# Optimization experiments

Measured on AMD Instinct MI355X. Metric: run time of the kernel, lower is better.

The kernel has to match this reference:

```python
import jax, jax.numpy as jnp
import numpy as np

RNN = 64      # rnn_hidden_dim
HID = 64      # hidden_dim
ENC = 3       # encoder_dim
NAG = 8       # n_agents
NACT = 14     # n_actions
CLIP = 0.2    # args.exp_clip (variance floor)
BN_EPS = 1e-5


def _bn(x, g, b):
    # BatchNorm1d in training mode: batch stats, biased variance
    m = x.mean(0)
    v = jnp.mean((x - m) ** 2, 0)
    return g * (x - m) * jax.lax.rsqrt(v + BN_EPS) + b


def setup_inputs() -> dict:
    key = jax.random.key(0)
    ks = jax.random.split(key, 16)
    B, INP = 8192, 96

    def w(k, shape, fan):
        return (jax.random.normal(k, shape, jnp.float32) / np.float32(np.sqrt(fan)))

    d = {}
    d["inputs"] = jax.random.normal(ks[0], (B * NAG, INP), jnp.float32)
    d["hidden_state"] = jax.random.normal(ks[1], (B * NAG, RNN), jnp.float32)
    d["noise"] = jax.random.normal(ks[2], (B, NAG, NAG * ENC), jnp.float32)
    d["fc1_w"] = w(ks[3], (INP, RNN), INP); d["fc1_b"] = jnp.zeros((RNN,), jnp.float32)
    d["w_ih"] = w(ks[4], (RNN, 3 * RNN), RNN); d["w_hh"] = w(ks[5], (RNN, 3 * RNN), RNN)
    d["b_ih"] = jnp.zeros((3 * RNN,), jnp.float32); d["b_hh"] = jnp.zeros((3 * RNN,), jnp.float32)
    d["aw1_w"] = w(ks[6], (RNN, HID), RNN); d["aw1_b"] = jnp.zeros((HID,), jnp.float32)
    d["aw_g"] = jnp.ones((HID,), jnp.float32); d["aw_be"] = jnp.zeros((HID,), jnp.float32)
    d["aw2_w"] = w(ks[7], (HID, 2 * NAG * ENC), HID); d["aw2_b"] = jnp.zeros((2 * NAG * ENC,), jnp.float32)
    d["po1_w"] = w(ks[8], (2 * RNN, HID), 2 * RNN); d["po1_b"] = jnp.zeros((HID,), jnp.float32)
    d["po_g"] = jnp.ones((HID,), jnp.float32); d["po_be"] = jnp.zeros((HID,), jnp.float32)
    d["po2_w"] = w(ks[9], (HID, 2 * ENC), HID); d["po2_b"] = jnp.zeros((2 * ENC,), jnp.float32)
    d["fc2_w"] = w(ks[10], (RNN + ENC * NAG, NACT), RNN + ENC * NAG); d["fc2_b"] = jnp.zeros((NACT,), jnp.float32)
    return d


def reference(inputs, hidden_state, noise,
              fc1_w, fc1_b, w_ih, w_hh, b_ih, b_hh,
              aw1_w, aw1_b, aw_g, aw_be, aw2_w, aw2_b,
              po1_w, po1_b, po_g, po_be, po2_w, po2_b,
              fc2_w, fc2_b):
    B, n, enc = noise.shape[0], NAG, ENC

    x = jax.nn.relu(inputs @ fc1_w + fc1_b)                      # [B*n, RNN]
    h_in = hidden_state.reshape(-1, RNN)

    # torch GRUCell
    gi = x @ w_ih + b_ih
    gh = h_in @ w_hh + b_hh
    ir, iz, i_n = jnp.split(gi, 3, axis=-1)
    hr, hz, h_n = jnp.split(gh, 3, axis=-1)
    r = jax.nn.sigmoid(ir + hr)
    z = jax.nn.sigmoid(iz + hz)
    nt = jnp.tanh(i_n + r * h_n)
    h = (1.0 - z) * nt + z * h_in                                # [B*n, RNN]

    # awareness encoder
    a = jax.nn.relu(_bn(h @ aw1_w + aw1_b, aw_g, aw_be))
    aw = (a @ aw2_w + aw2_b).reshape(B, n, 2 * n * enc)
    mu = aw[:, :, : n * enc]
    sigma = jnp.maximum(jnp.exp(aw[:, :, n * enc:]), CLIP)       # variance
    c = (mu + jnp.sqrt(sigma) * noise).reshape(-1, n * enc)      # rsample

    x_out = jnp.concatenate([h, c], axis=-1) @ fc2_w + fc2_b     # [B*n, NACT]

    # poster branch (training mode): all-pairs concat H[b, j, id] = [h[b,id], h[b,j]]
    hd = jax.lax.stop_gradient(h).reshape(B, n, RNN)
    Hi = jnp.broadcast_to(hd[:, None, :, :], (B, n, n, RNN))     # axis2 = id
    Hj = jnp.broadcast_to(hd[:, :, None, :], (B, n, n, RNN))     # axis1 = j
    H = jnp.concatenate([Hi, Hj], axis=-1).reshape(-1, 2 * RNN)  # [B*n*n, 2*RNN]

    p = jax.nn.relu(_bn(H @ po1_w + po1_b, po_g, po_be))
    out = (p @ po2_w + po2_b).reshape(B, n, 2 * n * enc)
    mu1 = out[:, :, : n * enc]
    sigma1 = jnp.maximum(jnp.exp(out[:, :, n * enc:]), CLIP)

    # KL between diagonal Gaussians (sigma, sigma1 are variances)
    kl = 0.5 * (jnp.log(sigma1 / sigma) + (sigma + (mu - mu1) ** 2) / sigma1 - 1.0)
    KL = kl.mean(axis=-1).mean(axis=-1, keepdims=True)           # [B, 1]
    return (x_out, h, KL)
```

## Files before the change

### kernel.cpp

```cpp
#include <hip/hip_runtime.h>
#include <math.h>

#define NROWS 65536
#define NB    8192
#define STAT_OFF  0
#define WPACK_OFF 448
#define OUT_XOUT 0
#define OUT_H    917504
#define OUT_KL   5111808

typedef __attribute__((ext_vector_type(8))) short bhalf8;
typedef __attribute__((ext_vector_type(4))) float floatx4;
typedef __attribute__((ext_vector_type(4))) unsigned short u16x4;

__device__ __forceinline__ float sigmf(float x) { return 1.0f / (1.0f + __expf(-x)); }
__device__ __forceinline__ float tanhfast(float x) {
    x = fminf(fmaxf(x, -15.f), 15.f);
    float e = __expf(-2.f * x);
    return (1.f - e) / (1.f + e);
}
__device__ __forceinline__ unsigned short f2bf(float f) {
    unsigned int u = __float_as_uint(f);
    u += 0x7FFFu + ((u >> 16) & 1u);
    return (unsigned short)(u >> 16);
}
__device__ __forceinline__ float bf2f(unsigned short s) {
    return __uint_as_float(((unsigned int)s) << 16);
}
__device__ __forceinline__ bhalf8 pack8(float4 a, float4 b) {
    bhalf8 r;
    r[0] = (short)f2bf(a.x); r[1] = (short)f2bf(a.y);
    r[2] = (short)f2bf(a.z); r[3] = (short)f2bf(a.w);
    r[4] = (short)f2bf(b.x); r[5] = (short)f2bf(b.y);
    r[6] = (short)f2bf(b.z); r[7] = (short)f2bf(b.w);
    return r;
}

__device__ __forceinline__ int p2idx(int g, int i) {
    switch (i) {
        case 0:  return (0 + g) * 2 + 0;   case 1:  return (0 + g) * 2 + 1;
        case 2:  return (12 + g) * 2 + 0;  case 3:  return (12 + g) * 2 + 1;
        case 4:  return (4 + g) * 2 + 0;   case 5:  return (4 + g) * 2 + 1;
        case 6:  return (16 + g) * 2 + 0;  case 7:  return (16 + g) * 2 + 1;
        case 8:  return (8 + g) * 2 + 0;   case 9:  return (8 + g) * 2 + 1;
        case 10: return (20 + g) * 2 + 0;  default: return (20 + g) * 2 + 1;
    }
}
__device__ __forceinline__ int p3idx(int g, int i) {
    switch (i) {
        case 0: return g * 2 + 0;        case 1: return g * 2 + 1;
        case 2: return (4 + g) * 2 + 0;  case 3: return (4 + g) * 2 + 1;
        case 4: return (8 + g) * 2 + 0;  default: return (8 + g) * 2 + 1;
    }
}

__global__ void k_prep(const float* __restrict__ fc1_w,
                       const float* __restrict__ w_ih, const float* __restrict__ w_hh,
                       const float* __restrict__ aw1_w, const float* __restrict__ po1_w,
                       const float* __restrict__ aw2_w, const float* __restrict__ fc2_w,
                       float* __restrict__ ws)
{
    const int t = threadIdx.x;
    if (blockIdx.x == 0)
        for (int i = t; i < 448; i += 256) ws[STAT_OFF + i] = 0.f;

    unsigned short* wpk = (unsigned short*)(ws + WPACK_OFF);
    for (int f = blockIdx.x * 256 + t; f < 5952; f += gridDim.x * 256) {
        int lane, c, tile;
        const float* src;
        int colbase, krowstride, kofs = 0, kmax = 1 << 30, colmax = 16;
        if (f < 768) {
            tile = f / 192; c = (f % 192) / 64; lane = f % 64;
            src = fc1_w; krowstride = 64; colbase = tile * 16;
        } else if (f < 3840) {
            int f2 = f - 768;
            tile = f2 / 128; c = (f2 % 128) / 64; lane = f2 % 64;
            if (tile < 12) { src = w_ih; colbase = tile * 16; }
            else           { src = w_hh; colbase = (tile - 12) * 16; }
            krowstride = 192;
        } else if (f < 5376) {
            int f3 = f - 3840;
            tile = f3 / 128; c = (f3 % 128) / 64; lane = f3 % 64;
            if (tile < 4)       { src = aw1_w; colbase = tile * 16; }
            else if (tile < 8)  { src = po1_w; colbase = (tile - 4) * 16; }
            else                { src = po1_w; colbase = (tile - 8) * 16; kofs = 64; }
            krowstride = 64;
        } else if (f < 5760) {
            int f4 = f - 5376;
            tile = f4 / 128; c = (f4 % 128) / 64; lane = f4 % 64;
            src = aw2_w; krowstride = 48; colbase = tile * 16;
        } else {
            int f5 = f - 5760;
            c = f5 / 64; lane = f5 % 64;
            src = fc2_w; krowstride = 14; colbase = 0;
            kmax = 88; colmax = 14;
        }
        int n = lane & 15, quad = lane >> 4;
        int col = colbase + n;
        unsigned short o[8];
        #pragma unroll
        for (int j = 0; j < 8; j++) {
            int k = c * 32 + quad * 8 + j + kofs;
            float v = (k < kmax && n < colmax) ? src[(size_t)k * krowstride + col] : 0.f;
            o[j] = f2bf(v);
        }
        u16x4 lo, hi;
        lo.x = o[0]; lo.y = o[1]; lo.z = o[2]; lo.w = o[3];
        hi.x = o[4]; hi.y = o[5]; hi.z = o[6]; hi.w = o[7];
        *(u16x4*)&wpk[f * 8]     = lo;
        *(u16x4*)&wpk[f * 8 + 4] = hi;
    }
}

__global__ __launch_bounds__(256, 2) void k_front(
    const float* __restrict__ inp, const float* __restrict__ hin,
    const float* __restrict__ fc1_b,
    const float* __restrict__ b_ih, const float* __restrict__ b_hh,
    const float* __restrict__ aw1_b,
    float* __restrict__ h_out, float* __restrict__ ws)
{
    __shared__ __align__(16) unsigned short s_xb[128 * 80];
    __shared__ float s_stat[448];

    const int t = threadIdx.x;
    const int row0 = blockIdx.x * 128;
    const int lane = t & 63;
    const int w = t >> 6;
    const int n16 = lane & 15;
    const int quad = lane >> 4;

    for (int i = t; i < 448; i += 256) s_stat[i] = 0.f;
    __syncthreads();

    const bhalf8* wp1 = (const bhalf8*)((const unsigned short*)(ws + WPACK_OFF));
    const bhalf8* wp2 = wp1 + 768;
    const bhalf8* wp3 = wp1 + 3840;

    bhalf8 ai[2][3], ahf[2][2];
    #pragma unroll
    for (int u = 0; u < 2; u++) {
        const float* gi = inp + (size_t)(row0 + w * 32 + u * 16 + n16) * 96 + quad * 8;
        #pragma unroll
        for (int kc = 0; kc < 3; kc++)
            ai[u][kc] = pack8(*(const float4*)&gi[kc * 32], *(const float4*)&gi[kc * 32 + 4]);
        const float* gh = hin + (size_t)(row0 + w * 32 + u * 16 + n16) * 64 + quad * 8;
        #pragma unroll
        for (int kc = 0; kc < 2; kc++)
            ahf[u][kc] = pack8(*(const float4*)&gh[kc * 32], *(const float4*)&gh[kc * 32 + 4]);
    }

    float b1v[4], brv[4], bzv[4], binv[4], bhnv[4], abv[4];
    #pragma unroll
    for (int g = 0; g < 4; g++) {
        int col = g * 16 + n16;
        b1v[g]  = fc1_b[col];
        brv[g]  = b_ih[col] + b_hh[col];
        bzv[g]  = b_ih[64 + col] + b_hh[64 + col];
        binv[g] = b_ih[128 + col];
        bhnv[g] = b_hh[128 + col];
        abv[g]  = aw1_b[col];
    }

    bhalf8 f1a[2][3];
    #pragma unroll
    for (int i = 0; i < 3; i++) f1a[0][i] = wp1[i * 64 + lane];
    #pragma unroll
    for (int g = 0; g < 4; g++) {
        const int cur = g & 1, nxt = cur ^ 1;
        if (g < 3) {
            #pragma unroll
            for (int i = 0; i < 3; i++) f1a[nxt][i] = wp1[((g + 1) * 3 + i) * 64 + lane];
        }
        int col = g * 16 + n16;
        #pragma unroll
        for (int u = 0; u < 2; u++) {
            floatx4 d = {0.f, 0.f, 0.f, 0.f};
            d = __builtin_amdgcn_mfma_f32_16x16x32_bf16(ai[u][0], f1a[cur][0], d, 0, 0, 0);
            d = __builtin_amdgcn_mfma_f32_16x16x32_bf16(ai[u][1], f1a[cur][1], d, 0, 0, 0);
            d = __builtin_amdgcn_mfma_f32_16x16x32_bf16(ai[u][2], f1a[cur][2], d, 0, 0, 0);
            #pragma unroll
            for (int q = 0; q < 4; q++)
                s_xb[(w * 32 + u * 16 + quad * 4 + q) * 80 + col] = f2bf(fmaxf(d[q] + b1v[g], 0.f));
        }
    }

    bhalf8 f2a[2][12];
    float hpv[2][8];
    #pragma unroll
    for (int i = 0; i < 12; i++) f2a[0][i] = wp2[p2idx(0, i) * 64 + lane];
    #pragma unroll
    for (int u = 0; u < 2; u++)
        #pragma unroll
        for (int q = 0; q < 4; q++)
            hpv[0][u * 4 + q] = hin[(size_t)(row0 + w * 32 + u * 16 + quad * 4 + q) * 64 + n16];

    bhalf8 ax[2][2];
    #pragma unroll
    for (int u = 0; u < 2; u++) {
        int mr = w * 32 + u * 16 + n16;
        ax[u][0] = *(const bhalf8*)&s_xb[mr * 80 + 0  + quad * 8];
        ax[u][1] = *(const bhalf8*)&s_xb[mr * 80 + 32 + quad * 8];
    }

    #pragma unroll
    for (int g = 0; g < 4; g++) {
        const int cur = g & 1, nxt = cur ^ 1;
        if (g < 3) {
            #pragma unroll
            for (int i = 0; i < 12; i++) f2a[nxt][i] = wp2[p2idx(g + 1, i) * 64 + lane];
            #pragma unroll
            for (int u = 0; u < 2; u++)
                #pragma unroll
                for (int q = 0; q < 4; q++)
                    hpv[nxt][u * 4 + q] = hin[(size_t)(row0 + w * 32 + u * 16 + quad * 4 + q) * 64 + (g + 1) * 16 + n16];
        }
        int col = g * 16 + n16;
        floatx4 dr[2], dz[2], dn[2], dh[2];
        #pragma unroll
        for (int u = 0; u < 2; u++) {
            floatx4 d = {0.f, 0.f, 0.f, 0.f};
            d = __builtin_amdgcn_mfma_f32_16x16x32_bf16(ax[u][0], f2a[cur][0], d, 0, 0, 0);
            d = __builtin_amdgcn_mfma_f32_16x16x32_bf16(ax[u][1], f2a[cur][1], d, 0, 0, 0);
            d = __builtin_amdgcn_mfma_f32_16x16x32_bf16(ahf[u][0], f2a[cur][2], d, 0, 0, 0);
            d = __builtin_amdgcn_mfma_f32_16x16x32_bf16(ahf[u][1], f2a[cur][3], d, 0, 0, 0);
            dr[u] = d;
            floatx4 e = {0.f, 0.f, 0.f, 0.f};
            e = __builtin_amdgcn_mfma_f32_16x16x32_bf16(ax[u][0], f2a[cur][4], e, 0, 0, 0);
            e = __builtin_amdgcn_mfma_f32_16x16x32_bf16(ax[u][1], f2a[cur][5], e, 0, 0, 0);
            e = __builtin_amdgcn_mfma_f32_16x16x32_bf16(ahf[u][0], f2a[cur][6], e, 0, 0, 0);
            e = __builtin_amdgcn_mfma_f32_16x16x32_bf16(ahf[u][1], f2a[cur][7], e, 0, 0, 0);
            dz[u] = e;
            floatx4 f = {0.f, 0.f, 0.f, 0.f};
            f = __builtin_amdgcn_mfma_f32_16x16x32_bf16(ax[u][0], f2a[cur][8], f, 0, 0, 0);
            f = __builtin_amdgcn_mfma_f32_16x16x32_bf16(ax[u][1], f2a[cur][9], f, 0, 0, 0);
            dn[u] = f;
            floatx4 h4 = {0.f, 0.f, 0.f, 0.f};
            h4 = __builtin_amdgcn_mfma_f32_16x16x32_bf16(ahf[u][0], f2a[cur][10], h4, 0, 0, 0);
            h4 = __builtin_amdgcn_mfma_f32_16x16x32_bf16(ahf[u][1], f2a[cur][11], h4, 0, 0, 0);
            dh[u] = h4;
        }
        #pragma unroll
        for (int u = 0; u < 2; u++) {
            #pragma unroll
            for (int q = 0; q < 4; q++) {
                int lrow = w * 32 + u * 16 + quad * 4 + q;
                size_t grow = (size_t)(row0 + lrow);
                float r  = sigmf(dr[u][q] + brv[g]);
                float z  = sigmf(dz[u][q] + bzv[g]);
                float nt = tanhfast(dn[u][q] + binv[g] + r * (dh[u][q] + bhnv[g]));
                float hp = hpv[cur][u * 4 + q];
                float h  = (1.f - z) * nt + z * hp;
                h_out[grow * 64 + col] = h;
                s_xb[lrow * 80 + col] = f2bf(h);
            }
        }
    }

    bhalf8 f3a[2][6];
    #pragma unroll
    for (int i = 0; i < 6; i++) f3a[0][i] = wp3[p3idx(0, i) * 64 + lane];

    bhalf8 hh[2][2];
    #pragma unroll
    for (int u = 0; u < 2; u++) {
        int mr = w * 32 + u * 16 + n16;
        hh[u][0] = *(const bhalf8*)&s_xb[mr * 80 + 0  + quad * 8];
        hh[u][1] = *(const bhalf8*)&s_xb[mr * 80 + 32 + quad * 8];
    }

    #pragma unroll
    for (int g = 0; g < 4; g++) {
        const int cur = g & 1, nxt = cur ^ 1;
        if (g < 3) {
            #pragma unroll
            for (int i = 0; i < 6; i++) f3a[nxt][i] = wp3[p3idx(g + 1, i) * 64 + lane];
        }
        int col = g * 16 + n16;
        floatx4 da[2], du[2], dvv[2];
        #pragma unroll
        for (int u = 0; u < 2; u++) {
            floatx4 d = {0.f, 0.f, 0.f, 0.f};
            d = __builtin_amdgcn_mfma_f32_16x16x32_bf16(hh[u][0], f3a[cur][0], d, 0, 0, 0);
            d = __builtin_amdgcn_mfma_f32_16x16x32_bf16(hh[u][1], f3a[cur][1], d, 0, 0, 0);
            da[u] = d;
            floatx4 e = {0.f, 0.f, 0.f, 0.f};
            e = __builtin_amdgcn_mfma_f32_16x16x32_bf16(hh[u][0], f3a[cur][2], e, 0, 0, 0);
            e = __builtin_amdgcn_mfma_f32_16x16x32_bf16(hh[u][1], f3a[cur][3], e, 0, 0, 0);
            du[u] = e;
            floatx4 f = {0.f, 0.f, 0.f, 0.f};
            f = __builtin_amdgcn_mfma_f32_16x16x32_bf16(hh[u][0], f3a[cur][4], f, 0, 0, 0);
            f = __builtin_amdgcn_mfma_f32_16x16x32_bf16(hh[u][1], f3a[cur][5], f, 0, 0, 0);
            dvv[u] = f;
        }
        float ab = abv[g];
        float s1 = 0.f, s2 = 0.f, suq = 0.f, svq = 0.f;
        float su[2] = {0.f, 0.f}, sv[2] = {0.f, 0.f};
        #pragma unroll
        for (int u = 0; u < 2; u++) {
            #pragma unroll
            for (int q = 0; q < 4; q++) {
                float a = da[u][q] + ab; s1 += a; s2 += a * a;
                float uv = du[u][q]; su[u] += uv; suq += uv * uv;
                float vv = dvv[u][q]; sv[u] += vv; svq += vv * vv;
            }
        }
        #pragma unroll
        for (int u = 0; u < 2; u++) {
            float u8 = su[u] + __shfl_xor(su[u], 16, 64);
            float v8 = sv[u] + __shfl_xor(sv[u], 16, 64);
            if ((quad & 1) == 0)
                atomicAdd(&s_stat[384 + col], u8 * v8 * (1.f / 64.f));
        }
        float sut = su[0] + su[1];
        float svt = sv[0] + sv[1];
        float t1 = s1 + __shfl_xor(s1, 16, 64);   t1 += __shfl_xor(t1, 32, 64);
        float t2 = s2 + __shfl_xor(s2, 16, 64);   t2 += __shfl_xor(t2, 32, 64);
        float t3 = sut + __shfl_xor(sut, 16, 64); t3 += __shfl_xor(t3, 32, 64);
        float t4 = suq + __shfl_xor(suq, 16, 64); t4 += __shfl_xor(t4, 32, 64);
        float t5 = svt + __shfl_xor(svt, 16, 64); t5 += __shfl_xor(t5, 32, 64);
        float t6 = svq + __shfl_xor(svq, 16, 64); t6 += __shfl_xor(t6, 32, 64);
        if (quad == 0) {
            atomicAdd(&s_stat[col], t1);
            atomicAdd(&s_stat[64 + col], t2);
            atomicAdd(&s_stat[128 + col], t3);
            atomicAdd(&s_stat[192 + col], t4);
            atomicAdd(&s_stat[256 + col], t5);
            atomicAdd(&s_stat[320 + col], t6);
        }
    }
    __syncthreads();
    if (t < 64) {
        float* gs = ws + STAT_OFF;
        #pragma unroll
        for (int q = 0; q < 7; q++)
            atomicAdd(&gs[q * 64 + t], s_stat[q * 64 + t]);
    }
}

__global__ __launch_bounds__(128) void k_heads(
    const float* __restrict__ h_glob, const float* __restrict__ noise,
    const float* __restrict__ aw1_b, const float* __restrict__ aw2_b,
    const float* __restrict__ fc2_b, const float* __restrict__ po2_b,
    const float* __restrict__ aw_g, const float* __restrict__ aw_be,
    const float* __restrict__ po_g, const float* __restrict__ po_be,
    const float* __restrict__ po1_b, const float* __restrict__ po2_w,
    const float* __restrict__ ws, float* __restrict__ out)
{
    __shared__ __align__(16) unsigned short s_hb[32 * 104];
    __shared__ __align__(16) unsigned short s_Ub[32 * 80];
    __shared__ __align__(16) unsigned short s_Vb[32 * 80];
    __shared__ float s_ms[32 * 48];
    __shared__ __align__(16) float s_out[32 * 48];
    __shared__ __align__(16) float s_dv[640];
    __shared__ float s_kl[32];

    const int t = threadIdx.x;
    const int row0 = blockIdx.x * 32;
    const int b0 = blockIdx.x * 4;
    const int lane = t & 63;
    const int w = t >> 6;
    const int n16 = lane & 15;
    const int quad = lane >> 4;
    const int mrow = w * 16 + n16;

    if (t < 64) {
        const float* st = ws + STAT_OFF;
        const float invN = 1.f / 65536.f;
        float am = st[t] * invN;
        float av = st[64 + t] * invN - am * am;
        float asc = aw_g[t] * rsqrtf(av + 1e-5f);
        s_dv[t] = asc;
        s_dv[64 + t] = aw_be[t] - asc * am;
        float Eu = st[128 + t] * invN;
        float vu = st[192 + t] * invN - Eu * Eu;
        float Ev = st[256 + t] * invN;
        float vv = st[320 + t] * invN - Ev * Ev;
        float cov = st[384 + t] * (1.f / 8192.f) - Eu * Ev;
        float my = Eu + Ev + po1_b[t];
        float vy = vu + vv + 2.f * cov;
        float psc = po_g[t] * rsqrtf(vy + 1e-5f);
        s_dv[128 + t] = psc;
        s_dv[192 + t] = po_be[t] + psc * (po1_b[t] - my);
    }
    for (int i = t; i < 384; i += 128) {
        int d = i >> 6, c = i & 63;
        s_dv[256 + i] = po2_w[c * 6 + d];
    }

    {
        const float* gh = h_glob + (size_t)row0 * 64;
        for (int i = t; i < 512; i += 128) {
            int r = i >> 4, c4 = (i & 15) * 4;
            float4 v = *(const float4*)&gh[r * 64 + c4];
            u16x4 p; p.x = f2bf(v.x); p.y = f2bf(v.y); p.z = f2bf(v.z); p.w = f2bf(v.w);
            *(u16x4*)&s_hb[r * 104 + c4] = p;
        }
        for (int i = t; i < 64; i += 128) {
            int r = i >> 1, c4 = 88 + (i & 1) * 4;
            u16x4 z; z.x = 0; z.y = 0; z.z = 0; z.w = 0;
            *(u16x4*)&s_hb[r * 104 + c4] = z;
        }
    }
    __syncthreads();

    const bhalf8* wp3  = ((const bhalf8*)((const unsigned short*)(ws + WPACK_OFF))) + 3840;
    const bhalf8* wpa2 = wp3 + 1536;
    const bhalf8* wpf2 = wpa2 + 384;
    unsigned short* s_ab = (unsigned short*)s_out;

    {
        bhalf8 ah0 = *(const bhalf8*)&s_hb[mrow * 104 + 0  + quad * 8];
        bhalf8 ah1 = *(const bhalf8*)&s_hb[mrow * 104 + 32 + quad * 8];
        #pragma unroll
        for (int g = 0; g < 4; g++) {
            int col = g * 16 + n16;
            floatx4 da = {0.f, 0.f, 0.f, 0.f}, duu = {0.f, 0.f, 0.f, 0.f}, dvv = {0.f, 0.f, 0.f, 0.f};
            da  = __builtin_amdgcn_mfma_f32_16x16x32_bf16(ah0, wp3[(g * 2 + 0) * 64 + lane], da, 0, 0, 0);
            da  = __builtin_amdgcn_mfma_f32_16x16x32_bf16(ah1, wp3[(g * 2 + 1) * 64 + lane], da, 0, 0, 0);
            duu = __builtin_amdgcn_mfma_f32_16x16x32_bf16(ah0, wp3[((4 + g) * 2 + 0) * 64 + lane], duu, 0, 0, 0);
            duu = __builtin_amdgcn_mfma_f32_16x16x32_bf16(ah1, wp3[((4 + g) * 2 + 1) * 64 + lane], duu, 0, 0, 0);
            dvv = __builtin_amdgcn_mfma_f32_16x16x32_bf16(ah0, wp3[((8 + g) * 2 + 0) * 64 + lane], dvv, 0, 0, 0);
            dvv = __builtin_amdgcn_mfma_f32_16x16x32_bf16(ah1, wp3[((8 + g) * 2 + 1) * 64 + lane], dvv, 0, 0, 0);
            float ab = aw1_b[col];
            float asc = s_dv[col], ash = s_dv[64 + col];
            float psc = s_dv[128 + col], psh = s_dv[192 + col];
            #pragma unroll
            for (int q = 0; q < 4; q++) {
                int lrow = w * 16 + quad * 4 + q;
                s_ab[lrow * 80 + col] = f2bf(fmaxf(asc * (da[q] + ab) + ash, 0.f));
                s_Ub[lrow * 80 + col] = f2bf(psc * duu[q]);
                s_Vb[lrow * 80 + col] = f2bf(psc * dvv[q] + psh);
            }
        }
    }

    {
        bhalf8 aa0 = *(const bhalf8*)&s_ab[mrow * 80 + 0  + quad * 8];
        bhalf8 aa1 = *(const bhalf8*)&s_ab[mrow * 80 + 32 + quad * 8];
        #pragma unroll
        for (int g = 0; g < 3; g++) {
            floatx4 d = {0.f, 0.f, 0.f, 0.f};
            d = __builtin_amdgcn_mfma_f32_16x16x32_bf16(aa0, wpa2[(g * 2 + 0) * 64 + lane], d, 0, 0, 0);
            d = __builtin_amdgcn_mfma_f32_16x16x32_bf16(aa1, wpa2[(g * 2 + 1) * 64 + lane], d, 0, 0, 0);
            int col = g * 16 + n16;
            float bb = aw2_b[col];
            #pragma unroll
            for (int q = 0; q < 4; q++) {
                int lrow = w * 16 + quad * 4 + q;
                float v = d[q] + bb;
                s_ms[lrow * 48 + col] = (col < 24) ? v : fmaxf(__expf(v), 0.2f);
            }
        }
    }
    __syncthreads();

    for (int i = t; i < 768; i += 128) {
        int r = i / 24, m = i - r * 24;
        float c = s_ms[r * 48 + m] + sqrtf(s_ms[r * 48 + 24 + m]) * noise[(size_t)(row0 + r) * 24 + m];
        s_hb[r * 104 + 64 + m] = f2bf(c);
    }
    __syncthreads();

    {
        bhalf8 hc0 = *(const bhalf8*)&s_hb[mrow * 104 + 0  + quad * 8];
        bhalf8 hc1 = *(const bhalf8*)&s_hb[mrow * 104 + 32 + quad * 8];
        bhalf8 hc2 = *(const bhalf8*)&s_hb[mrow * 104 + 64 + quad * 8];
        floatx4 d = {0.f, 0.f, 0.f, 0.f};
        d = __builtin_amdgcn_mfma_f32_16x16x32_bf16(hc0, wpf2[0 * 64 + lane], d, 0, 0, 0);
        d = __builtin_amdgcn_mfma_f32_16x16x32_bf16(hc1, wpf2[1 * 64 + lane], d, 0, 0, 0);
        d = __builtin_amdgcn_mfma_f32_16x16x32_bf16(hc2, wpf2[2 * 64 + lane], d, 0, 0, 0);
        if (n16 < 14) {
            float bb = fc2_b[n16];
            float* xout = out + OUT_XOUT;
            #pragma unroll
            for (int q = 0; q < 4; q++) {
                size_t grow = (size_t)(row0 + w * 16 + quad * 4 + q);
                xout[grow * 14 + n16] = d[q] + bb;
            }
        }
    }
    __syncthreads();

    {
        const float* p2t = s_dv + 256;
        const int bl = t >> 5;
        const int rem = t & 31;
        const int i_ = rem >> 2;
        const int j0 = (rem & 3) * 2;
        float acc[2][6];
        #pragma unroll
        for (int jj = 0; jj < 2; jj++)
            #pragma unroll
            for (int d = 0; d < 6; d++) acc[jj][d] = 0.f;

        for (int c = 0; c < 64; c += 4) {
            u16x4 vb4 = *(const u16x4*)&s_Vb[(bl * 8 + i_) * 80 + c];
            float vv[4] = {bf2f(vb4.x), bf2f(vb4.y), bf2f(vb4.z), bf2f(vb4.w)};
            float wv[6][4];
            #pragma unroll
            for (int d = 0; d < 6; d++) *(float4*)wv[d] = *(const float4*)&p2t[d * 64 + c];
            #pragma unroll
            for (int jj = 0; jj < 2; jj++) {
                u16x4 ub4 = *(const u16x4*)&s_Ub[(bl * 8 + j0 + jj) * 80 + c];
                float p[4];
                p[0] = fmaxf(bf2f(ub4.x) + vv[0], 0.f);
                p[1] = fmaxf(bf2f(ub4.y) + vv[1], 0.f);
                p[2] = fmaxf(bf2f(ub4.z) + vv[2], 0.f);
                p[3] = fmaxf(bf2f(ub4.w) + vv[3], 0.f);
                #pragma unroll
                for (int d = 0; d < 6; d++)
                    acc[jj][d] += p[0] * wv[d][0] + p[1] * wv[d][1] + p[2] * wv[d][2] + p[3] * wv[d][3];
            }
        }
        #pragma unroll
        for (int jj = 0; jj < 2; jj++)
            #pragma unroll
            for (int d = 0; d < 6; d++)
                s_out[(bl * 8 + i_) * 48 + (j0 + jj) * 6 + d] = acc[jj][d] + po2_b[d];
    }
    __syncthreads();

    if (t < 32) {
        float s = 0.f;
        #pragma unroll 4
        for (int m = 0; m < 24; m++) {
            float mu0 = s_ms[t * 48 + m];
            float sg0 = s_ms[t * 48 + 24 + m];
            float mu1 = s_out[t * 48 + m];
            float sg1 = fmaxf(__expf(s_out[t * 48 + 24 + m]), 0.2f);
            float d0 = mu0 - mu1;
            s += __logf(sg1 / sg0) + (sg0 + d0 * d0) / sg1 - 1.f;
        }
        s_kl[t] = s;
    }
    __syncthreads();
    if (t < 4) {
        float s = 0.f;
        #pragma unroll
        for (int i = 0; i < 8; i++) s += s_kl[t * 8 + i];
        out[OUT_KL + b0 + t] = s * (0.5f / 192.f);
    }
}

extern "C" void kernel_launch(void* const* d_in, const int* in_sizes, int n_in,
                              void* d_out, int out_size, void* d_ws, size_t ws_size,
                              hipStream_t stream)
{
    (void)in_sizes; (void)n_in; (void)out_size; (void)ws_size;
    const float* inp   = (const float*)d_in[0];
    const float* hin   = (const float*)d_in[1];
    const float* noise = (const float*)d_in[2];
    const float* fc1_w = (const float*)d_in[3];
    const float* fc1_b = (const float*)d_in[4];
    const float* w_ih  = (const float*)d_in[5];
    const float* w_hh  = (const float*)d_in[6];
    const float* b_ih  = (const float*)d_in[7];
    const float* b_hh  = (const float*)d_in[8];
    const float* aw1_w = (const float*)d_in[9];
    const float* aw1_b = (const float*)d_in[10];
    const float* aw_g  = (const float*)d_in[11];
    const float* aw_be = (const float*)d_in[12];
    const float* aw2_w = (const float*)d_in[13];
    const float* aw2_b = (const float*)d_in[14];
    const float* po1_w = (const float*)d_in[15];
    const float* po1_b = (const float*)d_in[16];
    const float* po_g  = (const float*)d_in[17];
    const float* po_be = (const float*)d_in[18];
    const float* po2_w = (const float*)d_in[19];
    const float* po2_b = (const float*)d_in[20];
    const float* fc2_w = (const float*)d_in[21];
    const float* fc2_b = (const float*)d_in[22];
    float* out = (float*)d_out;
    float* ws  = (float*)d_ws;

    hipLaunchKernelGGL(k_prep,  dim3(24),   dim3(256), 0, stream,
                       fc1_w, w_ih, w_hh, aw1_w, po1_w, aw2_w, fc2_w, ws);
    hipLaunchKernelGGL(k_front, dim3(512),  dim3(256), 0, stream,
                       inp, hin, fc1_b, b_ih, b_hh, aw1_b, out + OUT_H, ws);
    hipLaunchKernelGGL(k_heads, dim3(2048), dim3(128), 0, stream,
                       out + OUT_H, noise, aw1_b, aw2_b, fc2_b, po2_b,
                       aw_g, aw_be, po_g, po_be, po1_b, po2_w, ws, out);
}
```

Measured before the change: 188.1 us.

## Shard BN stat atomics, prefetch MFMA weight fragments, reshape prep launch

Result: faster. 181.8 us (-3.3%).

```diff
diff --git a/kernel.cpp b/kernel.cpp
--- a/kernel.cpp
+++ b/kernel.cpp
@@ -4,7 +4,7 @@
 #define NROWS 65536
 #define NB    8192
 #define STAT_OFF  0
-#define WPACK_OFF 448
+#define WPACK_OFF 3584
 #define OUT_XOUT 0
 #define OUT_H    917504
 #define OUT_KL   5111808
@@ -62,10 +62,11 @@
 {
     const int t = threadIdx.x;
     if (blockIdx.x == 0)
-        for (int i = t; i < 448; i += 256) ws[STAT_OFF + i] = 0.f;
+        for (int i = t; i < 3584; i += 64) ws[STAT_OFF + i] = 0.f;
 
     unsigned short* wpk = (unsigned short*)(ws + WPACK_OFF);
-    for (int f = blockIdx.x * 256 + t; f < 5952; f += gridDim.x * 256) {
+    int f = blockIdx.x * 64 + t;
+    if (f < 5952) {
         int lane, c, tile;
         const float* src;
         int colbase, krowstride, kofs = 0, kmax = 1 << 30, colmax = 16;
@@ -330,7 +331,7 @@
     }
     __syncthreads();
     if (t < 64) {
-        float* gs = ws + STAT_OFF;
+        float* gs = ws + STAT_OFF + (blockIdx.x & 7) * 448;
         #pragma unroll
         for (int q = 0; q < 7; q++)
             atomicAdd(&gs[q * 64 + t], s_stat[q * 64 + t]);
@@ -365,17 +366,25 @@
 
     if (t < 64) {
         const float* st = ws + STAT_OFF;
+        float sa = 0.f, sb = 0.f, sc = 0.f, sd = 0.f, se = 0.f, sf = 0.f, sg = 0.f;
+        #pragma unroll
+        for (int r = 0; r < 8; r++) {
+            const float* sr = st + r * 448;
+            sa += sr[t];       sb += sr[64 + t];  sc += sr[128 + t];
+            sd += sr[192 + t]; se += sr[256 + t]; sf += sr[320 + t];
+            sg += sr[384 + t];
+        }
         const float invN = 1.f / 65536.f;
-        float am = st[t] * invN;
-        float av = st[64 + t] * invN - am * am;
+        float am = sa * invN;
+        float av = sb * invN - am * am;
         float asc = aw_g[t] * rsqrtf(av + 1e-5f);
         s_dv[t] = asc;
         s_dv[64 + t] = aw_be[t] - asc * am;
-        float Eu = st[128 + t] * invN;
-        float vu = st[192 + t] * invN - Eu * Eu;
-        float Ev = st[256 + t] * invN;
-        float vv = st[320 + t] * invN - Ev * Ev;
-        float cov = st[384 + t] * (1.f / 8192.f) - Eu * Ev;
+        float Eu = sc * invN;
+        float vu = sd * invN - Eu * Eu;
+        float Ev = se * invN;
+        float vv = sf * invN - Ev * Ev;
+        float cov = sg * (1.f / 8192.f) - Eu * Ev;
         float my = Eu + Ev + po1_b[t];
         float vy = vu + vv + 2.f * cov;
         float psc = po_g[t] * rsqrtf(vy + 1e-5f);
@@ -386,6 +395,14 @@
         int d = i >> 6, c = i & 63;
         s_dv[256 + i] = po2_w[c * 6 + d];
     }
+
+    const bhalf8* wp3  = ((const bhalf8*)((const unsigned short*)(ws + WPACK_OFF))) + 3840;
+    const bhalf8* wpa2 = wp3 + 1536;
+    const bhalf8* wpf2 = wpa2 + 384;
+
+    float abv[4];
+    #pragma unroll
+    for (int g = 0; g < 4; g++) abv[g] = aw1_b[g * 16 + n16];
 
     {
         const float* gh = h_glob + (size_t)row0 * 64;
@@ -401,57 +418,86 @@
             *(u16x4*)&s_hb[r * 104 + c4] = z;
         }
     }
-    __syncthreads();
-
-    const bhalf8* wp3  = ((const bhalf8*)((const unsigned short*)(ws + WPACK_OFF))) + 3840;
-    const bhalf8* wpa2 = wp3 + 1536;
-    const bhalf8* wpf2 = wpa2 + 384;
+
+    bhalf8 fA[2][6];
+    #pragma unroll
+    for (int i = 0; i < 6; i++) fA[0][i] = wp3[p3idx(0, i) * 64 + lane];
+
+    __syncthreads();
+
     unsigned short* s_ab = (unsigned short*)s_out;
+
+    float ascv[4], ashv[4], pscv[4], pshv[4];
+    #pragma unroll
+    for (int g = 0; g < 4; g++) {
+        int col = g * 16 + n16;
+        ascv[g] = s_dv[col];       ashv[g] = s_dv[64 + col];
+        pscv[g] = s_dv[128 + col]; pshv[g] = s_dv[192 + col];
+    }
 
     {
         bhalf8 ah0 = *(const bhalf8*)&s_hb[mrow * 104 + 0  + quad * 8];
         bhalf8 ah1 = *(const bhalf8*)&s_hb[mrow * 104 + 32 + quad * 8];
         #pragma unroll
         for (int g = 0; g < 4; g++) {
+            const int cur = g & 1, nxt = cur ^ 1;
+            if (g < 3) {
+                #pragma unroll
+                for (int i = 0; i < 6; i++) fA[nxt][i] = wp3[p3idx(g + 1, i) * 64 + lane];
+            }
             int col = g * 16 + n16;
             floatx4 da = {0.f, 0.f, 0.f, 0.f}, duu = {0.f, 0.f, 0.f, 0.f}, dvv = {0.f, 0.f, 0.f, 0.f};
-            da  = __builtin_amdgcn_mfma_f32_16x16x32_bf16(ah0, wp3[(g * 2 + 0) * 64 + lane], da, 0, 0, 0);
-            da  = __builtin_amdgcn_mfma_f32_16x16x32_bf16(ah1, wp3[(g * 2 + 1) * 64 + lane], da, 0, 0, 0);
-            duu = __builtin_amdgcn_mfma_f32_16x16x32_bf16(ah0, wp3[((4 + g) * 2 + 0) * 64 + lane], duu, 0, 0, 0);
-            duu = __builtin_amdgcn_mfma_f32_16x16x32_bf16(ah1, wp3[((4 + g) * 2 + 1) * 64 + lane], duu, 0, 0, 0);
-            dvv = __builtin_amdgcn_mfma_f32_16x16x32_bf16(ah0, wp3[((8 + g) * 2 + 0) * 64 + lane], dvv, 0, 0, 0);
-            dvv = __builtin_amdgcn_mfma_f32_16x16x32_bf16(ah1, wp3[((8 + g) * 2 + 1) * 64 + lane], dvv, 0, 0, 0);
-            float ab = aw1_b[col];
-            float asc = s_dv[col], ash = s_dv[64 + col];
-            float psc = s_dv[128 + col], psh = s_dv[192 + col];
+            da  = __builtin_amdgcn_mfma_f32_16x16x32_bf16(ah0, fA[cur][0], da, 0, 0, 0);
+            da  = __builtin_amdgcn_mfma_f32_16x16x32_bf16(ah1, fA[cur][1], da, 0, 0, 0);
+            duu = __builtin_amdgcn_mfma_f32_16x16x32_bf16(ah0, fA[cur][2], duu, 0, 0, 0);
+            duu = __builtin_amdgcn_mfma_f32_16x16x32_bf16(ah1, fA[cur][3], duu, 0, 0, 0);
+            dvv = __builtin_amdgcn_mfma_f32_16x16x32_bf16(ah0, fA[cur][4], dvv, 0, 0, 0);
+            dvv = __builtin_amdgcn_mfma_f32_16x16x32_bf16(ah1, fA[cur][5], dvv, 0, 0, 0);
             #pragma unroll
             for (int q = 0; q < 4; q++) {
                 int lrow = w * 16 + quad * 4 + q;
-                s_ab[lrow * 80 + col] = f2bf(fmaxf(asc * (da[q] + ab) + ash, 0.f));
-                s_Ub[lrow * 80 + col] = f2bf(psc * duu[q]);
-                s_Vb[lrow * 80 + col] = f2bf(psc * dvv[q] + psh);
+                s_ab[lrow * 80 + col] = f2bf(fmaxf(ascv[g] * (da[q] + abv[g]) + ashv[g], 0.f));
+                s_Ub[lrow * 80 + col] = f2bf(pscv[g] * duu[q]);
+                s_Vb[lrow * 80 + col] = f2bf(pscv[g] * dvv[q] + pshv[g]);
             }
         }
     }
 
     {
+        bhalf8 fB[2][2];
+        fB[0][0] = wpa2[0 * 64 + lane];
+        fB[0][1] = wpa2[1 * 64 + lane];
+        float bbv[3];
+        #pragma unroll
+        for (int g = 0; g < 3; g++) bbv[g] = aw2_b[g * 16 + n16];
+
         bhalf8 aa0 = *(const bhalf8*)&s_ab[mrow * 80 + 0  + quad * 8];
         bhalf8 aa1 = *(const bhalf8*)&s_ab[mrow * 80 + 32 + quad * 8];
         #pragma unroll
         for (int g = 0; g < 3; g++) {
+            const int cur = g & 1, nxt = cur ^ 1;
+            if (g < 2) {
+                fB[nxt][0] = wpa2[((g + 1) * 2 + 0) * 64 + lane];
+                fB[nxt][1] = wpa2[((g + 1) * 2 + 1) * 64 + lane];
+            }
             floatx4 d = {0.f, 0.f, 0.f, 0.f};
-            d = __builtin_amdgcn_mfma_f32_16x16x32_bf16(aa0, wpa2[(g * 2 + 0) * 64 + lane], d, 0, 0, 0);
-            d = __builtin_amdgcn_mfma_f32_16x16x32_bf16(aa1, wpa2[(g * 2 + 1) * 64 + lane], d, 0, 0, 0);
+            d = __builtin_amdgcn_mfma_f32_16x16x32_bf16(aa0, fB[cur][0], d, 0, 0, 0);
+            d = __builtin_amdgcn_mfma_f32_16x16x32_bf16(aa1, fB[cur][1], d, 0, 0, 0);
             int col = g * 16 + n16;
-            float bb = aw2_b[col];
             #pragma unroll
             for (int q = 0; q < 4; q++) {
                 int lrow = w * 16 + quad * 4 + q;
-                float v = d[q] + bb;
+                float v = d[q] + bbv[g];
                 s_ms[lrow * 48 + col] = (col < 24) ? v : fmaxf(__expf(v), 0.2f);
             }
         }
     }
+
+    bhalf8 ff[3];
+    ff[0] = wpf2[0 * 64 + lane];
+    ff[1] = wpf2[1 * 64 + lane];
+    ff[2] = wpf2[2 * 64 + lane];
+
     __syncthreads();
 
     for (int i = t; i < 768; i += 128) {
@@ -466,9 +512,9 @@
         bhalf8 hc1 = *(const bhalf8*)&s_hb[mrow * 104 + 32 + quad * 8];
         bhalf8 hc2 = *(const bhalf8*)&s_hb[mrow * 104 + 64 + quad * 8];
         floatx4 d = {0.f, 0.f, 0.f, 0.f};
-        d = __builtin_amdgcn_mfma_f32_16x16x32_bf16(hc0, wpf2[0 * 64 + lane], d, 0, 0, 0);
-        d = __builtin_amdgcn_mfma_f32_16x16x32_bf16(hc1, wpf2[1 * 64 + lane], d, 0, 0, 0);
-        d = __builtin_amdgcn_mfma_f32_16x16x32_bf16(hc2, wpf2[2 * 64 + lane], d, 0, 0, 0);
+        d = __builtin_amdgcn_mfma_f32_16x16x32_bf16(hc0, ff[0], d, 0, 0, 0);
+        d = __builtin_amdgcn_mfma_f32_16x16x32_bf16(hc1, ff[1], d, 0, 0, 0);
+        d = __builtin_amdgcn_mfma_f32_16x16x32_bf16(hc2, ff[2], d, 0, 0, 0);
         if (n16 < 14) {
             float bb = fc2_b[n16];
             float* xout = out + OUT_XOUT;
@@ -573,7 +619,7 @@
     float* out = (float*)d_out;
     float* ws  = (float*)d_ws;
 
-    hipLaunchKernelGGL(k_prep,  dim3(24),   dim3(256), 0, stream,
+    hipLaunchKernelGGL(k_prep,  dim3(93),   dim3(64), 0, stream,
                        fc1_w, w_ih, w_hh, aw1_w, po1_w, aw2_w, fc2_w, ws);
     hipLaunchKernelGGL(k_front, dim3(512),  dim3(256), 0, stream,
                        inp, hin, fc1_b, b_ih, b_hh, aw1_b, out + OUT_H, ws);
```
